# Kernel tuning notes

Hardware: AMD Instinct MI355X
Metric: run time of the kernel (lower is better)

## Reference

```python
import jax, jax.numpy as jnp
import numpy as np

H, N, BSZ, L = 512, 64, 8, 2048
DT_MIN, DT_MAX = 1e-3, 1e-1


def _hippo_dplr(n_state):
    """HiPPO-LegS -> DPLR (Lambda, P, B) init, as in the Annotated S4."""
    n = np.arange(n_state, dtype=np.float64)
    p = np.sqrt(n + 0.5)                      # low-rank factor P
    pm = np.sqrt(1.0 + 2.0 * n)
    A = np.tril(pm[:, None] * pm[None, :]) - np.diag(n)
    A = -A                                    # HiPPO-LegS A
    S = A + p[:, None] * p[None, :]           # normal part (skew-symmetric + cI)
    lam_real = np.mean(np.diagonal(S)) * np.ones(n_state)
    lam_imag, V = np.linalg.eigh(S * -1j)
    Lam = lam_real + 1j * lam_imag
    B = np.sqrt(2.0 * n + 1.0)
    return Lam, V.conj().T @ p, V.conj().T @ B


def setup_inputs() -> dict:
    key = jax.random.key(0)
    k1, k2, k3, k4, k5 = jax.random.split(key, 5)
    Lam, P, B = _hippo_dplr(N)
    return {
        "u": jax.random.normal(k1, (BSZ, L, H), dtype=jnp.float32),
        "Lambda_real": jnp.asarray(Lam.real, jnp.float32),
        "Lambda_imag": jnp.asarray(Lam.imag, jnp.float32),
        "P_real": jnp.asarray(P.real, jnp.float32),
        "P_imag": jnp.asarray(P.imag, jnp.float32),
        "B_real": jnp.asarray(B.real, jnp.float32),
        "B_imag": jnp.asarray(B.imag, jnp.float32),
        "C_real": jax.random.normal(k2, (H, N), jnp.float32) * 0.5,
        "C_imag": jax.random.normal(k3, (H, N), jnp.float32) * 0.5,
        "log_dt": jax.random.uniform(k4, (H,), jnp.float32,
                                     float(np.log(DT_MIN)), float(np.log(DT_MAX))),
        "D": jax.random.normal(k5, (H,), jnp.float32) * 0.01,
    }


def _s4_forward(u, Lr, Li, Pr, Pi, Br, Bi, Cr, Ci, log_dt, D):
    Lam = (Lr + 1j * Li).astype(jnp.complex64)   # (N,)
    P = (Pr + 1j * Pi).astype(jnp.complex64)     # (N,)
    B = (Br + 1j * Bi).astype(jnp.complex64)     # (N,)
    C = (Cr + 1j * Ci).astype(jnp.complex64)     # (H, N)
    l_len = u.shape[1]
    dt = jnp.exp(log_dt)                         # (H,)

    # --- DPLR kernel via Cauchy-kernel generating function (bilinear disc),
    # batched over all H channels instead of the per-channel Python loop. ---
    omega = jnp.exp(-2j * jnp.pi * jnp.arange(l_len, dtype=jnp.float32) / l_len)
    omega = omega.astype(jnp.complex64)          # roots of unity, (L,)
    g = (2.0 / dt)[:, None].astype(jnp.complex64) * ((1.0 - omega) / (1.0 + omega))[None, :]  # (H, L)
    c2 = 2.0 / (1.0 + omega)                     # (L,)
    r = 1.0 / (g[:, :, None] - Lam[None, None, :])  # Cauchy resolvent (H, L, N)
    Cc = jnp.conj(C)                             # (H, N)
    Qc = jnp.conj(P)                             # (N,)
    k00 = jnp.einsum('hn,hln->hl', Cc * B[None, :], r)
    k01 = jnp.einsum('hn,hln->hl', Cc * P[None, :], r)
    k10 = jnp.einsum('n,hln->hl', Qc * B, r)
    k11 = jnp.einsum('n,hln->hl', Qc * P, r)
    at_roots = c2[None, :] * (k00 - k01 * k10 / (1.0 + k11))  # (H, L)
    K = jnp.fft.ifft(at_roots, axis=-1).real.astype(u.dtype)  # (H, L) conv kernel

    # --- causal FFT convolution per channel ---
    x = jnp.swapaxes(u, -1, -2)                  # (B, H, L)
    n_fft = 2 * l_len
    Xf = jnp.fft.rfft(x, n=n_fft)
    Kf = jnp.fft.rfft(K, n=n_fft)
    y = jnp.fft.irfft(Xf * Kf[None], n=n_fft)[..., :l_len]
    y = y + x * D[None, :, None]                 # skip connection
    return jnp.swapaxes(y, -1, -2)               # (B, L, H)


def reference(u, Lambda_real, Lambda_imag, P_real, P_imag, B_real, B_imag,
              C_real, C_imag, log_dt, D):
    return _s4_forward(u, Lambda_real, Lambda_imag, P_real, P_imag,
                       B_real, B_imag, C_real, C_imag, log_dt, D)
```

## Files before the change

### kernel.cpp

```cpp
#include <hip/hip_runtime.h>
#include <math.h>

#define LSEQ 2048
#define HCH  512
#define NST  64
#define NBATCH 8
#define PIf 3.14159265358979f

#define PHYS(i) ((i) + ((i) >> 3))
#define LDSN 2304

__device__ __forceinline__ float2 cmul(float2 a, float2 b) {
    return make_float2(a.x * b.x - a.y * b.y, a.x * b.y + a.y * b.x);
}
__device__ __forceinline__ float2 cadd(float2 a, float2 b) { return make_float2(a.x + b.x, a.y + b.y); }
__device__ __forceinline__ float2 csub(float2 a, float2 b) { return make_float2(a.x - b.x, a.y - b.y); }
__device__ __forceinline__ float2 csq(float2 a) { return make_float2(a.x * a.x - a.y * a.y, 2.f * a.x * a.y); }
template<int INV>
__device__ __forceinline__ float2 rot90(float2 a) {
    return INV ? make_float2(-a.y, a.x) : make_float2(a.y, -a.x);
}

template<int INV, int STAGE>
__device__ __forceinline__ void radix8_inplace(float2* __restrict__ buf, int tid)
{
    __syncthreads();
    float2 x0 = buf[PHYS(tid)];
    float2 x1 = buf[PHYS(tid + 256)];
    float2 x2 = buf[PHYS(tid + 512)];
    float2 x3 = buf[PHYS(tid + 768)];
    float2 x4 = buf[PHYS(tid + 1024)];
    float2 x5 = buf[PHYS(tid + 1280)];
    float2 x6 = buf[PHYS(tid + 1536)];
    float2 x7 = buf[PHYS(tid + 1792)];
    __syncthreads();

    const int Ns  = 1 << STAGE;
    const int lam = tid & (Ns - 1);
    const int G   = ((tid >> STAGE) << (STAGE + 3)) + lam;
    const float SGN = INV ? 1.f : -1.f;
    float sn, cs;
    __sincosf(SGN * (PIf / (float)(4 * Ns)) * (float)lam, &sn, &cs);
    const float2 T3 = make_float2(cs, sn);
    const float2 T2 = csq(T3);
    const float2 T1 = csq(T2);
    const float r2 = 0.70710678118f;
    const float2 U = cmul(T3, make_float2(r2, SGN * r2));
    float2 t;
    t = cmul(T1, x4); float2 a0 = cadd(x0, t), a4 = csub(x0, t);
    t = cmul(T1, x5); float2 a1 = cadd(x1, t), a5 = csub(x1, t);
    t = cmul(T1, x6); float2 a2 = cadd(x2, t), a6 = csub(x2, t);
    t = cmul(T1, x7); float2 a3 = cadd(x3, t), a7 = csub(x3, t);
    t = cmul(T2, a2);             float2 b0 = cadd(a0, t), b2 = csub(a0, t);
    t = cmul(T2, a3);             float2 b1 = cadd(a1, t), b3 = csub(a1, t);
    t = rot90<INV>(cmul(T2, a6)); float2 b4 = cadd(a4, t), b6 = csub(a4, t);
    t = rot90<INV>(cmul(T2, a7)); float2 b5 = cadd(a5, t), b7 = csub(a5, t);
    t = cmul(T3, b1);             buf[PHYS(G)]          = cadd(b0, t); buf[PHYS(G + 4 * Ns)] = csub(b0, t);
    t = rot90<INV>(cmul(T3, b3)); buf[PHYS(G + 2 * Ns)] = cadd(b2, t); buf[PHYS(G + 6 * Ns)] = csub(b2, t);
    t = cmul(U, b5);              buf[PHYS(G + Ns)]     = cadd(b4, t); buf[PHYS(G + 5 * Ns)] = csub(b4, t);
    t = rot90<INV>(cmul(U, b7));  buf[PHYS(G + 3 * Ns)] = cadd(b6, t); buf[PHYS(G + 7 * Ns)] = csub(b6, t);
}

template<int INV>
__device__ __forceinline__ void radix4_inplace(float2* __restrict__ buf, int tid)
{
    __syncthreads();
    const float SGN = INV ? 1.f : -1.f;
#pragma unroll
    for (int q = 0; q < 2; ++q) {
        const int j = tid + (q << 8);
        float2 A  = buf[PHYS(j)];
        float2 C  = buf[PHYS(j + 512)];
        float2 B  = buf[PHYS(j + 1024)];
        float2 Dd = buf[PHYS(j + 1536)];
        float sn, cs;
        __sincosf(SGN * (PIf / 1024.f) * (float)j, &sn, &cs);
        const float2 v = make_float2(cs, sn);
        const float2 w = csq(v);
        float2 t = cmul(w, B);  float2 m1 = cadd(A, t), m2 = csub(A, t);
        t = cmul(w, Dd);        float2 m3 = cadd(C, t), m4 = csub(C, t);
        const float2 t3 = cmul(v, m3);
        const float2 t4 = rot90<INV>(cmul(v, m4));
        buf[PHYS(j)]        = cadd(m1, t3);
        buf[PHYS(j + 1024)] = csub(m1, t3);
        buf[PHYS(j + 512)]  = cadd(m2, t4);
        buf[PHYS(j + 1536)] = csub(m2, t4);
    }
}

template<int INV>
__device__ __forceinline__ void fft2048_ip(float2* buf, int tid)
{
    radix8_inplace<INV, 0>(buf, tid);
    radix8_inplace<INV, 3>(buf, tid);
    radix8_inplace<INV, 6>(buf, tid);
    radix4_inplace<INV>(buf, tid);
}

template<int INV, int STAGE>
__device__ __forceinline__ void radix4_ip512(float2* __restrict__ buf, int tid)
{
    __syncthreads();
    float2 x0 = buf[PHYS(tid)];
    float2 x1 = buf[PHYS(tid + 512)];
    float2 x2 = buf[PHYS(tid + 1024)];
    float2 x3 = buf[PHYS(tid + 1536)];
    __syncthreads();

    const int Ns  = 1 << STAGE;
    const int lam = tid & (Ns - 1);
    const int G   = ((tid >> STAGE) << (STAGE + 2)) + lam;
    const float SGN = INV ? 1.f : -1.f;
    float sn, cs;
    __sincosf(SGN * (PIf / (float)(2 * Ns)) * (float)lam, &sn, &cs);
    const float2 T2 = make_float2(cs, sn);
    const float2 T1 = csq(T2);
    float2 t;
    t = cmul(T1, x2); float2 b0 = cadd(x0, t), b1 = csub(x0, t);
    t = cmul(T1, x3); float2 b2 = cadd(x1, t), b3 = csub(x1, t);
    const float2 t2 = cmul(T2, b2);
    const float2 t3 = rot90<INV>(cmul(T2, b3));
    buf[PHYS(G)]          = cadd(b0, t2);
    buf[PHYS(G + 2 * Ns)] = csub(b0, t2);
    buf[PHYS(G + Ns)]     = cadd(b1, t3);
    buf[PHYS(G + 3 * Ns)] = csub(b1, t3);
}

template<int INV>
__device__ __forceinline__ void radix2_ip512(float2* __restrict__ buf, int tid)
{
    __syncthreads();
    const float SGN = INV ? 1.f : -1.f;
#pragma unroll
    for (int q = 0; q < 2; ++q) {
        const int j = tid + (q << 9);
        float2 A = buf[PHYS(j)];
        float2 B = buf[PHYS(j + 1024)];
        float sn, cs;
        __sincosf(SGN * (PIf / 1024.f) * (float)j, &sn, &cs);
        const float2 t = cmul(make_float2(cs, sn), B);
        buf[PHYS(j)]        = cadd(A, t);
        buf[PHYS(j + 1024)] = csub(A, t);
    }
}

template<int INV>
__device__ __forceinline__ void fft2048_ip512(float2* buf, int tid)
{
    radix4_ip512<INV, 0>(buf, tid);
    radix4_ip512<INV, 2>(buf, tid);
    radix4_ip512<INV, 4>(buf, tid);
    radix4_ip512<INV, 6>(buf, tid);
    radix4_ip512<INV, 8>(buf, tid);
    radix2_ip512<INV>(buf, tid);
}

__global__ __launch_bounds__(256, 4)
void s4_cauchy_kernel(const float* __restrict__ Lr, const float* __restrict__ Li,
                      const float* __restrict__ Pr, const float* __restrict__ Pi,
                      const float* __restrict__ Br, const float* __restrict__ Bi,
                      const float* __restrict__ Cr, const float* __restrict__ Ci,
                      const float* __restrict__ log_dt, float2* __restrict__ at_out)
{
    __shared__ float4 F0[NST];
    __shared__ float4 F1[NST];
    __shared__ float  q1s[NST];

    const int h    = blockIdx.x >> 1;
    const int half = blockIdx.x & 1;
    const int tid  = threadIdx.x;

    if (tid < NST) {
        const float pr = Pr[tid], pi = Pi[tid], br = Br[tid], bi = Bi[tid];
        const float cr = Cr[h * NST + tid], ci = Ci[h * NST + tid];
        F0[tid]  = make_float4(Lr[tid], Li[tid], cr * br + ci * bi, cr * bi - ci * br);
        F1[tid]  = make_float4(cr * pr + ci * pi, cr * pi - ci * pr,
                               pr * br + pi * bi, pr * bi - pi * br);
        q1s[tid] = pr * pr + pi * pi;
    }
    __syncthreads();

    const float dt = expf(log_dt[h]);
    const float a  = 2.0f / dt;

    float tt[4], g[4];
#pragma unroll
    for (int p = 0; p < 4; ++p) {
        const int l = (half << 10) + (p << 8) + tid;
        tt[p] = tanf(PIf * (float)l * (1.0f / 2048.0f));
        g[p]  = a * tt[p];
    }

    float k00r[4], k00i[4], k01r[4], k01i[4];
    float k10r[4], k10i[4], k11r[4], k11i[4];
#pragma unroll
    for (int p = 0; p < 4; ++p) {
        k00r[p] = 0.f; k00i[p] = 0.f; k01r[p] = 0.f; k01i[p] = 0.f;
        k10r[p] = 0.f; k10i[p] = 0.f; k11r[p] = 0.f; k11i[p] = 0.f;
    }

#pragma unroll 2
    for (int n = 0; n < NST; ++n) {
        const float4 f0 = F0[n];
        const float4 f1 = F1[n];
        const float q1 = q1s[n];
        const float x  = -f0.x;
        const float x2 = x * x;
#pragma unroll
        for (int p = 0; p < 4; ++p) {
            const float y   = g[p] - f0.y;
            const float inv = __builtin_amdgcn_rcpf(fmaf(y, y, x2));
            const float rr  = x * inv;
            const float ri  = -y * inv;
            k00r[p] = fmaf(f0.z, rr, fmaf(-f0.w, ri, k00r[p]));
            k00i[p] = fmaf(f0.z, ri, fmaf( f0.w, rr, k00i[p]));
            k01r[p] = fmaf(f1.x, rr, fmaf(-f1.y, ri, k01r[p]));
            k01i[p] = fmaf(f1.x, ri, fmaf( f1.y, rr, k01i[p]));
            k10r[p] = fmaf(f1.z, rr, fmaf(-f1.w, ri, k10r[p]));
            k10i[p] = fmaf(f1.z, ri, fmaf( f1.w, rr, k10i[p]));
            k11r[p] = fmaf(q1, rr, k11r[p]);
            k11i[p] = fmaf(q1, ri, k11i[p]);
        }
    }

    float2* __restrict__ row = at_out + (size_t)h * 2048;
#pragma unroll
    for (int p = 0; p < 4; ++p) {
        const int l = (half << 10) + (p << 8) + tid;
        const float dr = 1.0f + k11r[p], di = k11i[p];
        const float dinv = __builtin_amdgcn_rcpf(fmaf(dr, dr, di * di));
        const float pr_ = k01r[p] * k10r[p] - k01i[p] * k10i[p];
        const float pi_ = k01r[p] * k10i[p] + k01i[p] * k10r[p];
        const float qr = (pr_ * dr + pi_ * di) * dinv;
        const float qi = (pi_ * dr - pr_ * di) * dinv;
        const float sr = k00r[p] - qr, si = k00i[p] - qi;
        row[l] = make_float2(fmaf(-tt[p], si, sr), fmaf(tt[p], sr, si));
    }
}

__global__ __launch_bounds__(512, 4)
void s4_kf_kernel(const float2* __restrict__ at_in, float2* __restrict__ Kf)
{
    __shared__ float2 buf[LDSN];

    const int h   = blockIdx.x;
    const int tid = threadIdx.x;
    const float2* __restrict__ at = at_in + (size_t)h * 2048;

#pragma unroll
    for (int q = 0; q < 4; ++q) {
        const int l = tid + (q << 9);
        buf[PHYS(l)] = at[l];
    }

    fft2048_ip512<1>(buf, tid);

    __syncthreads();
    float re[2], im[2];
#pragma unroll
    for (int q = 0; q < 2; ++q) {
        const int n = tid + (q << 9);
        re[q] = buf[PHYS(2 * n)].x;
        im[q] = buf[PHYS(2 * n + 1)].x;
    }
    __syncthreads();
    const float sc = 1.0f / 2048.0f;
#pragma unroll
    for (int q = 0; q < 2; ++q) {
        const int n = tid + (q << 9);
        buf[PHYS(n)]        = make_float2(re[q] * sc, im[q] * sc);
        buf[PHYS(n + 1024)] = make_float2(0.f, 0.f);
    }

    fft2048_ip512<0>(buf, tid);
    __syncthreads();

    float2* __restrict__ out = Kf + (size_t)h * 2049;
    for (int k = tid; k < 1024; k += 512) {
        const float2 Zk = buf[PHYS(k)];
        const float2 Zm = buf[PHYS((2048 - k) & 2047)];
        const float zer = 0.5f * (Zk.x + Zm.x), zei = 0.5f * (Zk.y - Zm.y);
        const float zdr = Zk.x - Zm.x,          zdi = Zk.y + Zm.y;
        const float zor = 0.5f * zdi,           zoi = -0.5f * zdr;
        float s, c;
        __sincosf(-PIf * (float)k * (1.0f / 2048.0f), &s, &c);
        const float txr = c * zor - s * zoi;
        const float txi = c * zoi + s * zor;
        out[k] = make_float2(zer + txr, zei + txi);
        if (k > 0) {
            out[2048 - k] = make_float2(zer - txr, txi - zei);
        } else {
            out[2048] = make_float2(Zk.x - Zk.y, 0.f);
        }
    }
    if (tid == 0) {
        const float2 z = buf[PHYS(1024)];
        out[1024] = make_float2(z.x, -z.y);
    }
}

__global__ __launch_bounds__(256, 6)
void s4_conv_kernel(const float* __restrict__ u, float* ws_rows,
                    const float2* __restrict__ Kf, const float* __restrict__ Dv,
                    float* __restrict__ out, int fastpath)
{
    __shared__ float2 buf[LDSN];

    const int bh  = blockIdx.x;
    const int b   = bh >> 9;
    const int h   = bh & 511;
    const int tid = threadIdx.x;

    if (fastpath) {
        const float2* rowv = (const float2*)(ws_rows + (size_t)bh * LSEQ);
        for (int n = tid; n < 1024; n += 256) buf[PHYS(n)] = rowv[n];
    } else {
        const float* ub = u + (size_t)b * LSEQ * HCH + h;
        for (int n = tid; n < 1024; n += 256)
            buf[PHYS(n)] = make_float2(ub[(size_t)(2 * n) * HCH],
                                       ub[(size_t)(2 * n + 1) * HCH]);
    }
    for (int n = 1024 + tid; n < 2048; n += 256) buf[PHYS(n)] = make_float2(0.f, 0.f);

    fft2048_ip<0>(buf, tid);

    const float2* __restrict__ kf = Kf + (size_t)h * 2049;

    __syncthreads();
    float2 Zk[4], Zm[4], Z1024v;
#pragma unroll
    for (int q = 0; q < 4; ++q) {
        const int k = tid + (q << 8);
        Zk[q] = buf[PHYS(k)];
        Zm[q] = buf[PHYS((2048 - k) & 2047)];
    }
    if (tid == 0) Z1024v = buf[PHYS(1024)];
    __syncthreads();

#pragma unroll
    for (int q = 0; q < 4; ++q) {
        const int k = tid + (q << 8);
        const float2 zk = Zk[q], zm = Zm[q];
        const float zer = 0.5f * (zk.x + zm.x), zei = 0.5f * (zk.y - zm.y);
        const float zdr = zk.x - zm.x,          zdi = zk.y + zm.y;
        const float zor = 0.5f * zdi,           zoi = -0.5f * zdr;
        float s, c;
        __sincosf(-PIf * (float)k * (1.0f / 2048.0f), &s, &c);
        const float txr = c * zor - s * zoi;
        const float txi = c * zoi + s * zor;
        const float2 Xk = make_float2(zer + txr, zei + txi);
        float2 Yk = cmul(Xk, kf[k]);
        float2 Ym;
        if (k > 0) {
            const float2 Xm = make_float2(zer - txr, txi - zei);
            Ym = cmul(Xm, kf[2048 - k]);
        } else {
            const float x2048 = zk.x - zk.y;
            const float2 k2 = kf[2048];
            Ym = make_float2(x2048 * k2.x, x2048 * k2.y);
        }
        const float yer = 0.5f * (Yk.x + Ym.x), yei = 0.5f * (Yk.y - Ym.y);
        const float ydr = Yk.x - Ym.x,          ydi = Yk.y + Ym.y;
        const float yor = 0.5f * (c * ydr + s * ydi);
        const float yoi = 0.5f * (c * ydi - s * ydr);
        buf[PHYS(k)] = make_float2(yer - yoi, yei + yor);
        if (k > 0)
            buf[PHYS(2048 - k)] = make_float2(yer + yoi, yor - yei);
    }
    if (tid == 0) {
        const float2 kk = kf[1024];
        const float2 y = make_float2(Z1024v.x * kk.x + Z1024v.y * kk.y,
                                     Z1024v.x * kk.y - Z1024v.y * kk.x);
        buf[PHYS(1024)] = make_float2(y.x, -y.y);
    }

    fft2048_ip<1>(buf, tid);

    __syncthreads();
    const float Dh = Dv[h];
    const float sc = 1.0f / 2048.0f;
    if (fastpath) {
        float2* rowv = (float2*)(ws_rows + (size_t)bh * LSEQ);
        for (int n = tid; n < 1024; n += 256) {
            const float2 wv = buf[PHYS(n)];
            const float2 xv = rowv[n];
            rowv[n] = make_float2(wv.x * sc + Dh * xv.x,
                                  wv.y * sc + Dh * xv.y);
        }
    } else {
        const float* ub = u + (size_t)b * LSEQ * HCH + h;
        float* ob = out + (size_t)b * LSEQ * HCH + h;
        for (int n = tid; n < 1024; n += 256) {
            const float2 wv = buf[PHYS(n)];
            ob[(size_t)(2 * n) * HCH]     = wv.x * sc + Dh * ub[(size_t)(2 * n) * HCH];
            ob[(size_t)(2 * n + 1) * HCH] = wv.y * sc + Dh * ub[(size_t)(2 * n + 1) * HCH];
        }
    }
}

__global__ __launch_bounds__(256)
void transpose_kernel(const float* __restrict__ in, float* __restrict__ out,
                      int rows, int cols)
{
    __shared__ float tile[32][33];
    const int b  = blockIdx.z;
    const int r0 = blockIdx.y << 5;
    const int c0 = blockIdx.x << 5;
    const size_t base = (size_t)b * rows * cols;
    const int tx = threadIdx.x & 31;
    const int ty = threadIdx.x >> 5;
#pragma unroll
    for (int i = 0; i < 32; i += 8)
        tile[ty + i][tx] = in[base + (size_t)(r0 + ty + i) * cols + (c0 + tx)];
    __syncthreads();
#pragma unroll
    for (int i = 0; i < 32; i += 8)
        out[base + (size_t)(c0 + ty + i) * rows + (r0 + tx)] = tile[tx][ty + i];
}

extern "C" void kernel_launch(void* const* d_in, const int* in_sizes, int n_in,
                              void* d_out, int out_size, void* d_ws, size_t ws_size,
                              hipStream_t stream)
{
    (void)in_sizes; (void)n_in; (void)out_size;
    const float* u  = (const float*)d_in[0];
    const float* Lr = (const float*)d_in[1];
    const float* Li = (const float*)d_in[2];
    const float* Pr = (const float*)d_in[3];
    const float* Pi = (const float*)d_in[4];
    const float* Br = (const float*)d_in[5];
    const float* Bi = (const float*)d_in[6];
    const float* Cr = (const float*)d_in[7];
    const float* Ci = (const float*)d_in[8];
    const float* ld = (const float*)d_in[9];
    const float* Dv = (const float*)d_in[10];
    float* out = (float*)d_out;

    const size_t UT_BYTES = (size_t)NBATCH * HCH * LSEQ * sizeof(float);
    const size_t KF_BYTES = (size_t)HCH * 2049 * sizeof(float2);
    const int fast = (ws_size >= UT_BYTES + KF_BYTES) ? 1 : 0;

    float*  ut;
    float2* Kf;
    if (fast) { ut = (float*)d_ws; Kf = (float2*)((char*)d_ws + UT_BYTES); }
    else      { ut = (float*)d_ws; Kf = (float2*)d_ws; }

    float2* at = (float2*)d_out;

    hipLaunchKernelGGL(s4_cauchy_kernel, dim3(HCH * 2), dim3(256), 0, stream,
                       Lr, Li, Pr, Pi, Br, Bi, Cr, Ci, ld, at);
    hipLaunchKernelGGL(s4_kf_kernel, dim3(HCH), dim3(512), 0, stream, at, Kf);
    if (fast) {
        hipLaunchKernelGGL(transpose_kernel, dim3(HCH / 32, LSEQ / 32, NBATCH),
                           dim3(256), 0, stream, u, ut, LSEQ, HCH);
    }
    hipLaunchKernelGGL(s4_conv_kernel, dim3(NBATCH * HCH), dim3(256), 0, stream,
                       u, fast ? ut : nullptr, Kf, Dv, out, fast);
    if (fast) {
        hipLaunchKernelGGL(transpose_kernel, dim3(LSEQ / 32, HCH / 32, NBATCH),
                           dim3(256), 0, stream, ut, out, HCH, LSEQ);
    }
}
```

Baseline: 110.7 us.

## Fuse Cauchy evaluation into Kf FFT kernel and drop transpose passes

Merges the Cauchy-kernel evaluation with the inverse FFT that builds Kf, so each channel's spectrum stays in LDS instead of going through global memory. It also removes the two transpose kernels and the workspace fast path, and the conv kernel now always reads and writes u/out directly with strided (stride H) accesses. The fused block uses 512 threads at lower occupancy, and the strided global accesses may coalesce worse than the transposed layout did.

New measurement: 287.4 us. +159.6%, slower.

```diff
diff --git a/kernel.cpp b/kernel.cpp
--- a/kernel.cpp
+++ b/kernel.cpp
@@ -155,20 +155,20 @@
     radix2_ip512<INV>(buf, tid);
 }
 
-__global__ __launch_bounds__(256, 4)
-void s4_cauchy_kernel(const float* __restrict__ Lr, const float* __restrict__ Li,
-                      const float* __restrict__ Pr, const float* __restrict__ Pi,
-                      const float* __restrict__ Br, const float* __restrict__ Bi,
-                      const float* __restrict__ Cr, const float* __restrict__ Ci,
-                      const float* __restrict__ log_dt, float2* __restrict__ at_out)
-{
+__global__ __launch_bounds__(512, 2)
+void s4_kf_fused_kernel(const float* __restrict__ Lr, const float* __restrict__ Li,
+                        const float* __restrict__ Pr, const float* __restrict__ Pi,
+                        const float* __restrict__ Br, const float* __restrict__ Bi,
+                        const float* __restrict__ Cr, const float* __restrict__ Ci,
+                        const float* __restrict__ log_dt, float2* __restrict__ Kf)
+{
+    __shared__ float2 buf[LDSN];
     __shared__ float4 F0[NST];
     __shared__ float4 F1[NST];
     __shared__ float  q1s[NST];
 
-    const int h    = blockIdx.x >> 1;
-    const int half = blockIdx.x & 1;
-    const int tid  = threadIdx.x;
+    const int h   = blockIdx.x;
+    const int tid = threadIdx.x;
 
     if (tid < NST) {
         const float pr = Pr[tid], pi = Pi[tid], br = Br[tid], bi = Bi[tid];
@@ -186,7 +186,7 @@
     float tt[4], g[4];
 #pragma unroll
     for (int p = 0; p < 4; ++p) {
-        const int l = (half << 10) + (p << 8) + tid;
+        const int l = (p << 9) + tid;
         tt[p] = tanf(PIf * (float)l * (1.0f / 2048.0f));
         g[p]  = a * tt[p];
     }
@@ -223,10 +223,9 @@
         }
     }
 
-    float2* __restrict__ row = at_out + (size_t)h * 2048;
 #pragma unroll
     for (int p = 0; p < 4; ++p) {
-        const int l = (half << 10) + (p << 8) + tid;
+        const int l = (p << 9) + tid;
         const float dr = 1.0f + k11r[p], di = k11i[p];
         const float dinv = __builtin_amdgcn_rcpf(fmaf(dr, dr, di * di));
         const float pr_ = k01r[p] * k10r[p] - k01i[p] * k10i[p];
@@ -234,23 +233,7 @@
         const float qr = (pr_ * dr + pi_ * di) * dinv;
         const float qi = (pi_ * dr - pr_ * di) * dinv;
         const float sr = k00r[p] - qr, si = k00i[p] - qi;
-        row[l] = make_float2(fmaf(-tt[p], si, sr), fmaf(tt[p], sr, si));
-    }
-}
-
-__global__ __launch_bounds__(512, 4)
-void s4_kf_kernel(const float2* __restrict__ at_in, float2* __restrict__ Kf)
-{
-    __shared__ float2 buf[LDSN];
-
-    const int h   = blockIdx.x;
-    const int tid = threadIdx.x;
-    const float2* __restrict__ at = at_in + (size_t)h * 2048;
-
-#pragma unroll
-    for (int q = 0; q < 4; ++q) {
-        const int l = tid + (q << 9);
-        buf[PHYS(l)] = at[l];
+        buf[PHYS(l)] = make_float2(fmaf(-tt[p], si, sr), fmaf(tt[p], sr, si));
     }
 
     fft2048_ip512<1>(buf, tid);
@@ -300,9 +283,8 @@
 }
 
 __global__ __launch_bounds__(256, 6)
-void s4_conv_kernel(const float* __restrict__ u, float* ws_rows,
-                    const float2* __restrict__ Kf, const float* __restrict__ Dv,
-                    float* __restrict__ out, int fastpath)
+void s4_conv_kernel(const float* __restrict__ u, const float2* __restrict__ Kf,
+                    const float* __restrict__ Dv, float* __restrict__ out)
 {
     __shared__ float2 buf[LDSN];
 
@@ -311,15 +293,10 @@
     const int h   = bh & 511;
     const int tid = threadIdx.x;
 
-    if (fastpath) {
-        const float2* rowv = (const float2*)(ws_rows + (size_t)bh * LSEQ);
-        for (int n = tid; n < 1024; n += 256) buf[PHYS(n)] = rowv[n];
-    } else {
-        const float* ub = u + (size_t)b * LSEQ * HCH + h;
-        for (int n = tid; n < 1024; n += 256)
-            buf[PHYS(n)] = make_float2(ub[(size_t)(2 * n) * HCH],
-                                       ub[(size_t)(2 * n + 1) * HCH]);
-    }
+    const float* __restrict__ ub = u + (size_t)b * LSEQ * HCH + h;
+    for (int n = tid; n < 1024; n += 256)
+        buf[PHYS(n)] = make_float2(ub[(size_t)(2 * n) * HCH],
+                                   ub[(size_t)(2 * n + 1) * HCH]);
     for (int n = 1024 + tid; n < 2048; n += 256) buf[PHYS(n)] = make_float2(0.f, 0.f);
 
     fft2048_ip<0>(buf, tid);
@@ -379,50 +356,19 @@
     __syncthreads();
     const float Dh = Dv[h];
     const float sc = 1.0f / 2048.0f;
-    if (fastpath) {
-        float2* rowv = (float2*)(ws_rows + (size_t)bh * LSEQ);
-        for (int n = tid; n < 1024; n += 256) {
-            const float2 wv = buf[PHYS(n)];
-            const float2 xv = rowv[n];
-            rowv[n] = make_float2(wv.x * sc + Dh * xv.x,
-                                  wv.y * sc + Dh * xv.y);
-        }
-    } else {
-        const float* ub = u + (size_t)b * LSEQ * HCH + h;
-        float* ob = out + (size_t)b * LSEQ * HCH + h;
-        for (int n = tid; n < 1024; n += 256) {
-            const float2 wv = buf[PHYS(n)];
-            ob[(size_t)(2 * n) * HCH]     = wv.x * sc + Dh * ub[(size_t)(2 * n) * HCH];
-            ob[(size_t)(2 * n + 1) * HCH] = wv.y * sc + Dh * ub[(size_t)(2 * n + 1) * HCH];
-        }
-    }
-}
-
-__global__ __launch_bounds__(256)
-void transpose_kernel(const float* __restrict__ in, float* __restrict__ out,
-                      int rows, int cols)
-{
-    __shared__ float tile[32][33];
-    const int b  = blockIdx.z;
-    const int r0 = blockIdx.y << 5;
-    const int c0 = blockIdx.x << 5;
-    const size_t base = (size_t)b * rows * cols;
-    const int tx = threadIdx.x & 31;
-    const int ty = threadIdx.x >> 5;
-#pragma unroll
-    for (int i = 0; i < 32; i += 8)
-        tile[ty + i][tx] = in[base + (size_t)(r0 + ty + i) * cols + (c0 + tx)];
-    __syncthreads();
-#pragma unroll
-    for (int i = 0; i < 32; i += 8)
-        out[base + (size_t)(c0 + ty + i) * rows + (r0 + tx)] = tile[tx][ty + i];
+    float* __restrict__ ob = out + (size_t)b * LSEQ * HCH + h;
+    for (int n = tid; n < 1024; n += 256) {
+        const float2 wv = buf[PHYS(n)];
+        ob[(size_t)(2 * n) * HCH]     = wv.x * sc + Dh * ub[(size_t)(2 * n) * HCH];
+        ob[(size_t)(2 * n + 1) * HCH] = wv.y * sc + Dh * ub[(size_t)(2 * n + 1) * HCH];
+    }
 }
 
 extern "C" void kernel_launch(void* const* d_in, const int* in_sizes, int n_in,
                               void* d_out, int out_size, void* d_ws, size_t ws_size,
                               hipStream_t stream)
 {
-    (void)in_sizes; (void)n_in; (void)out_size;
+    (void)in_sizes; (void)n_in; (void)out_size; (void)ws_size;
     const float* u  = (const float*)d_in[0];
     const float* Lr = (const float*)d_in[1];
     const float* Li = (const float*)d_in[2];
@@ -436,28 +382,10 @@
     const float* Dv = (const float*)d_in[10];
     float* out = (float*)d_out;
 
-    const size_t UT_BYTES = (size_t)NBATCH * HCH * LSEQ * sizeof(float);
-    const size_t KF_BYTES = (size_t)HCH * 2049 * sizeof(float2);
-    const int fast = (ws_size >= UT_BYTES + KF_BYTES) ? 1 : 0;
-
-    float*  ut;
-    float2* Kf;
-    if (fast) { ut = (float*)d_ws; Kf = (float2*)((char*)d_ws + UT_BYTES); }
-    else      { ut = (float*)d_ws; Kf = (float2*)d_ws; }
-
-    float2* at = (float2*)d_out;
-
-    hipLaunchKernelGGL(s4_cauchy_kernel, dim3(HCH * 2), dim3(256), 0, stream,
-                       Lr, Li, Pr, Pi, Br, Bi, Cr, Ci, ld, at);
-    hipLaunchKernelGGL(s4_kf_kernel, dim3(HCH), dim3(512), 0, stream, at, Kf);
-    if (fast) {
-        hipLaunchKernelGGL(transpose_kernel, dim3(HCH / 32, LSEQ / 32, NBATCH),
-                           dim3(256), 0, stream, u, ut, LSEQ, HCH);
-    }
+    float2* Kf = (float2*)d_ws;
+
+    hipLaunchKernelGGL(s4_kf_fused_kernel, dim3(HCH), dim3(512), 0, stream,
+                       Lr, Li, Pr, Pi, Br, Bi, Cr, Ci, ld, Kf);
     hipLaunchKernelGGL(s4_conv_kernel, dim3(NBATCH * HCH), dim3(256), 0, stream,
-                       u, fast ? ut : nullptr, Kf, Dv, out, fast);
-    if (fast) {
-        hipLaunchKernelGGL(transpose_kernel, dim3(LSEQ / 32, HCH / 32, NBATCH),
-                           dim3(256), 0, stream, ut, out, HCH, LSEQ);
-    }
-}
+                       u, Kf, Dv, out);
+}
```
